# Kernel optimization log

Measured on AMD Instinct MI355X. Metric: run time of the kernel, lower is better.

The kernel has to match this reference:

```python
import jax, jax.numpy as jnp
import numpy as np

B, S, D, H = 2, 2048, 1024, 16
HEAD_DIM = D // H
WINDOW = 256
DILATION = 1
NEG = jnp.float32(-1e9)


def _build_attn_mask(seq_len):
    # Faithful port of torch _build_attn_mask for causal=True, stencil kind='local'.
    idx = jnp.arange(seq_len)
    diff = idx[None, :] - idx[:, None]  # diff[i, j] = j - i (torch diff is idx.unsqueeze(0)-idx.unsqueeze(1))
    # causal: -inf strictly above diagonal (j > i)
    mask = jnp.where(diff > 0, -jnp.inf, 0.0).astype(jnp.float32)
    # stencil allow: |diff| <= window and |diff| % dilation == 0
    cond = (jnp.abs(diff) <= WINDOW) & (jnp.abs(diff) % DILATION == 0)
    allowed = jnp.where(cond, 0.0, -jnp.inf).astype(jnp.float32)
    # torch.maximum: allow() can UNMASK causally-masked positions inside the window
    mask = jnp.maximum(mask, allowed)
    # clamp(min=-1e9)
    return jnp.maximum(mask, NEG)


def setup_inputs() -> dict:
    key = jax.random.key(0)
    k = jax.random.split(key, 5)
    return {
        "x": jax.random.normal(k[0], (B, S, D), dtype=jnp.float32),
        "in_proj_w": jax.random.normal(k[1], (3 * D, D), dtype=jnp.float32) * (D ** -0.5),
        "in_proj_b": jax.random.normal(k[2], (3 * D,), dtype=jnp.float32) * 0.02,
        "out_proj_w": jax.random.normal(k[3], (D, D), dtype=jnp.float32) * (D ** -0.5),
        "out_proj_b": jax.random.normal(k[4], (D,), dtype=jnp.float32) * 0.02,
    }


def reference(x, in_proj_w, in_proj_b, out_proj_w, out_proj_b):
    b, s, d = x.shape
    # fused qkv projection (torch nn.MultiheadAttention in_proj)
    qkv = x @ in_proj_w.T + in_proj_b  # [b, s, 3d]
    q, k, v = jnp.split(qkv, 3, axis=-1)

    def to_heads(t):
        return t.reshape(b, s, H, HEAD_DIM).transpose(0, 2, 1, 3)  # [b, h, s, hd]

    q, k, v = to_heads(q), to_heads(k), to_heads(v)
    scale = jnp.float32(HEAD_DIM) ** -0.5
    scores = jnp.einsum("bhqd,bhkd->bhqk", q * scale, k)  # [b, h, s, s]
    mask = _build_attn_mask(s)  # [s, s]
    scores = scores + mask[None, None, :, :]
    attn = jax.nn.softmax(scores, axis=-1)
    out = jnp.einsum("bhqk,bhkd->bhqd", attn, v)  # [b, h, s, hd]
    out = out.transpose(0, 2, 1, 3).reshape(b, s, d)
    return out @ out_proj_w.T + out_proj_b
```

## Files before the change

### kernel.cpp

```cpp
#include <hip/hip_runtime.h>
#include <cstddef>

#define BATCH   2
#define SEQ     2048
#define DMODEL  1024
#define NH      16
#define HDIM    64
#define WIN     256
#define MTOT    4096

typedef __bf16 bf16;
typedef __attribute__((ext_vector_type(8)))  __bf16 bf16x8;
typedef __attribute__((ext_vector_type(4)))  float  f32x4;
typedef __attribute__((ext_vector_type(16))) float  f32x16;

#define GLOAD_LDS(gp, lp) __builtin_amdgcn_global_load_lds( \
    (const __attribute__((address_space(1))) void*)(gp),    \
    (__attribute__((address_space(3))) void*)(lp), 16, 0, 0)

__device__ __forceinline__ float fast_exp2(float x) {
#if __has_builtin(__builtin_amdgcn_exp2f)
  return __builtin_amdgcn_exp2f(x);
#else
  float r; asm("v_exp_f32 %0, %1" : "=v"(r) : "v"(x)); return r;
#endif
}

__global__ __launch_bounds__(256)
void cvt_all(const float* __restrict__ x, const float* __restrict__ w1,
             const float* __restrict__ w2, bf16* __restrict__ xh,
             bf16* __restrict__ xl, bf16* __restrict__ w1h,
             bf16* __restrict__ w1l, bf16* __restrict__ w2h,
             bf16* __restrict__ w2l) {
  const int bid = blockIdx.x;
  const float* s; bf16 *hp, *lp; int base;
  if (bid < 2048)      { s = x;  hp = xh;  lp = xl;  base = bid * 2048; }
  else if (bid < 3584) { s = w1; hp = w1h; lp = w1l; base = (bid - 2048) * 2048; }
  else                 { s = w2; hp = w2h; lp = w2l; base = (bid - 3584) * 2048; }
  const int i = base + threadIdx.x * 8;
  float4 a = *(const float4*)(s + i);
  float4 c = *(const float4*)(s + i + 4);
  const float f[8] = {a.x, a.y, a.z, a.w, c.x, c.y, c.z, c.w};
  bf16x8 vh, vl;
#pragma unroll
  for (int j = 0; j < 8; ++j) {
    bf16 hh = (bf16)f[j];
    vh[j] = hh;
    vl[j] = (bf16)(f[j] - (float)hh);
  }
  *(bf16x8*)(hp + i) = vh;
  *(bf16x8*)(lp + i) = vl;
}

__global__ __launch_bounds__(256)
void gemm_qkv_fused(const bf16* __restrict__ xh, const bf16* __restrict__ xl,
                    const bf16* __restrict__ w1h, const bf16* __restrict__ w1l,
                    const float* __restrict__ b1,
                    bf16* __restrict__ Qh, bf16* __restrict__ Ql,
                    bf16* __restrict__ Kt, bf16* __restrict__ Vt) {
  __shared__ bf16 sAh[128 * 32];
  __shared__ bf16 sAl[128 * 32];
  __shared__ bf16 sBh[128 * 32];
  __shared__ bf16 sBl[128 * 32];

  const int t = threadIdx.x, w = t >> 6, lane = t & 63;
  const int ln15 = lane & 15, quad = lane >> 4;
  const int wrow = (w & 1) * 64, wcol = (w >> 1) * 64;
  const int drow = lane >> 2;
  const int dkcol = (lane & 3) * 8;
  const int bid = blockIdx.x;

  f32x4 acc[4][4];
#pragma unroll
  for (int i = 0; i < 4; ++i)
#pragma unroll
    for (int j = 0; j < 4; ++j)
#pragma unroll
      for (int r = 0; r < 4; ++r) acc[i][j][r] = 0.f;

  if (bid < 512) {
    const int bm = (bid >> 4) * 128;
    const int bnx = (bid & 15) ^ (((bid >> 8) & 1) << 3);
    const int bn = bnx * 128;
    const bool cross = (bn < 1024);

    for (int k0 = 0; k0 < DMODEL; k0 += 32) {
      __syncthreads();
#pragma unroll
      for (int half = 0; half < 2; ++half) {
        const int r = w * 32 + half * 16 + drow;
        const size_t goffA = (size_t)(bm + r) * DMODEL + k0 + dkcol;
        const size_t goffB = (size_t)(bn + r) * DMODEL + k0 + dkcol;
        const int loff = (w * 32 + half * 16) * 32;
        GLOAD_LDS(xh + goffA, sAh + loff);
        GLOAD_LDS(w1h + goffB, sBh + loff);
        if (cross) {
          GLOAD_LDS(xl + goffA, sAl + loff);
          GLOAD_LDS(w1l + goffB, sBl + loff);
        }
      }
      __syncthreads();

      bf16x8 afh[4], afl[4], bfh[4], bfl[4];
#pragma unroll
      for (int mt = 0; mt < 4; ++mt) {
        const int off = (wrow + mt * 16 + ln15) * 32 + quad * 8;
        afh[mt] = *(const bf16x8*)&sAh[off];
        if (cross) afl[mt] = *(const bf16x8*)&sAl[off];
      }
#pragma unroll
      for (int nt = 0; nt < 4; ++nt) {
        const int off = (wcol + nt * 16 + ln15) * 32 + quad * 8;
        bfh[nt] = *(const bf16x8*)&sBh[off];
        if (cross) bfl[nt] = *(const bf16x8*)&sBl[off];
      }
#pragma unroll
      for (int mt = 0; mt < 4; ++mt)
#pragma unroll
        for (int nt = 0; nt < 4; ++nt) {
          acc[mt][nt] = __builtin_amdgcn_mfma_f32_16x16x32_bf16(afh[mt], bfh[nt], acc[mt][nt], 0, 0, 0);
          if (cross) {
            acc[mt][nt] = __builtin_amdgcn_mfma_f32_16x16x32_bf16(afh[mt], bfl[nt], acc[mt][nt], 0, 0, 0);
            acc[mt][nt] = __builtin_amdgcn_mfma_f32_16x16x32_bf16(afl[mt], bfh[nt], acc[mt][nt], 0, 0, 0);
          }
        }
    }

    float bbcol[4];
#pragma unroll
    for (int nt = 0; nt < 4; ++nt) bbcol[nt] = b1[bn + wcol + nt * 16 + ln15];

#pragma unroll
    for (int mt = 0; mt < 4; ++mt)
#pragma unroll
      for (int r = 0; r < 4; ++r) {
        const size_t grow = (size_t)(bm + wrow + mt * 16 + quad * 4 + r);
#pragma unroll
        for (int nt = 0; nt < 4; ++nt) {
          const int col = bn + wcol + nt * 16 + ln15;
          const float v = acc[mt][nt][r] + bbcol[nt];
          if (col < 1024) {
            const bf16 hh = (bf16)v;
            Qh[grow * 1024 + col] = hh;
            Ql[grow * 1024 + col] = (bf16)(v - (float)hh);
          } else {
            const int btok = (int)(grow >> 11), key = (int)(grow & 2047);
            const int kt = key >> 6, kw = key & 63;
            const int hh2 = (col - 1024) >> 6, d = col & 63;
            const size_t addr = ((size_t)((btok * 16 + hh2) * 32 + kt) << 12)
                              + (((kw >> 5) * 4 + (d >> 4)) << 9)
                              + ((((d >> 3) & 1) << 5) + (kw & 31)) * 8 + (d & 7);
            Kt[addr] = (bf16)v;
          }
        }
      }
  } else {
    const int id = bid - 512;
    const int bm = (id >> 5) * 128, bn = (id & 31) * 128;
    const bf16* Ah = w1h + 2048 * 1024;
    const float* bias = b1 + 2048;

    for (int k0 = 0; k0 < DMODEL; k0 += 32) {
      __syncthreads();
#pragma unroll
      for (int half = 0; half < 2; ++half) {
        const int r = w * 32 + half * 16 + drow;
        const int loff = (w * 32 + half * 16) * 32;
        GLOAD_LDS(Ah + (size_t)(bm + r) * DMODEL + k0 + dkcol, sAh + loff);
        GLOAD_LDS(xh + (size_t)(bn + r) * DMODEL + k0 + dkcol, sBh + loff);
      }
      __syncthreads();

      bf16x8 af[4], bf[4];
#pragma unroll
      for (int mt = 0; mt < 4; ++mt)
        af[mt] = *(const bf16x8*)&sAh[(wrow + mt * 16 + ln15) * 32 + quad * 8];
#pragma unroll
      for (int nt = 0; nt < 4; ++nt)
        bf[nt] = *(const bf16x8*)&sBh[(wcol + nt * 16 + ln15) * 32 + quad * 8];
#pragma unroll
      for (int mt = 0; mt < 4; ++mt)
#pragma unroll
        for (int nt = 0; nt < 4; ++nt)
          acc[mt][nt] = __builtin_amdgcn_mfma_f32_16x16x32_bf16(af[mt], bf[nt], acc[mt][nt], 0, 0, 0);
    }

#pragma unroll
    for (int mt = 0; mt < 4; ++mt)
#pragma unroll
      for (int r = 0; r < 4; ++r) {
        const size_t grow = (size_t)(bm + wrow + mt * 16 + quad * 4 + r);
        const float brow = bias[grow];
        const int hh2 = (int)(grow >> 6), d = (int)(grow & 63);
#pragma unroll
        for (int nt = 0; nt < 4; ++nt) {
          const int col = bn + wcol + nt * 16 + ln15;
          const float v = acc[mt][nt][r] + brow;
          const int btok = col >> 11, key = col & 2047;
          const int kt = key >> 6, kw = key & 63;
          const size_t addr = ((size_t)((btok * 16 + hh2) * 32 + kt) << 12)
                            + (((d >> 5) * 4 + (kw >> 4)) << 9)
                            + ((((kw >> 3) & 1) << 5) + (d & 31)) * 8 + (kw & 7);
          Vt[addr] = (bf16)v;
        }
      }
  }
}

__global__ __launch_bounds__(256)
void gemm_out64(const bf16* __restrict__ Ah, const bf16* __restrict__ Al,
                const bf16* __restrict__ Bh, const bf16* __restrict__ Bl,
                const float* __restrict__ bias, float* __restrict__ Cf) {
  __shared__ bf16 sAh[64 * 32];
  __shared__ bf16 sAl[64 * 32];
  __shared__ bf16 sBh[64 * 32];
  __shared__ bf16 sBl[64 * 32];

  const int t = threadIdx.x, w = t >> 6, lane = t & 63;
  const int ln15 = lane & 15, quad = lane >> 4;
  const int bm = blockIdx.y * 64, bn = blockIdx.x * 64;
  const int wrow = (w & 1) * 32, wcol = (w >> 1) * 32;
  const int drow = lane >> 2;
  const int dkcol = (lane & 3) * 8;

  f32x4 acc[2][2];
#pragma unroll
  for (int i = 0; i < 2; ++i)
#pragma unroll
    for (int j = 0; j < 2; ++j)
#pragma unroll
      for (int r = 0; r < 4; ++r) acc[i][j][r] = 0.f;

  for (int k0 = 0; k0 < DMODEL; k0 += 32) {
    __syncthreads();
    {
      const int r = w * 16 + drow;
      const size_t goffA = (size_t)(bm + r) * DMODEL + k0 + dkcol;
      const size_t goffB = (size_t)(bn + r) * DMODEL + k0 + dkcol;
      const int loff = (w * 16) * 32;
      GLOAD_LDS(Ah + goffA, sAh + loff);
      GLOAD_LDS(Al + goffA, sAl + loff);
      GLOAD_LDS(Bh + goffB, sBh + loff);
      GLOAD_LDS(Bl + goffB, sBl + loff);
    }
    __syncthreads();

    bf16x8 afh[2], afl[2], bfh[2], bfl[2];
#pragma unroll
    for (int mt = 0; mt < 2; ++mt) {
      const int off = (wrow + mt * 16 + ln15) * 32 + quad * 8;
      afh[mt] = *(const bf16x8*)&sAh[off];
      afl[mt] = *(const bf16x8*)&sAl[off];
    }
#pragma unroll
    for (int nt = 0; nt < 2; ++nt) {
      const int off = (wcol + nt * 16 + ln15) * 32 + quad * 8;
      bfh[nt] = *(const bf16x8*)&sBh[off];
      bfl[nt] = *(const bf16x8*)&sBl[off];
    }
#pragma unroll
    for (int mt = 0; mt < 2; ++mt)
#pragma unroll
      for (int nt = 0; nt < 2; ++nt) {
        acc[mt][nt] = __builtin_amdgcn_mfma_f32_16x16x32_bf16(afh[mt], bfh[nt], acc[mt][nt], 0, 0, 0);
        acc[mt][nt] = __builtin_amdgcn_mfma_f32_16x16x32_bf16(afh[mt], bfl[nt], acc[mt][nt], 0, 0, 0);
        acc[mt][nt] = __builtin_amdgcn_mfma_f32_16x16x32_bf16(afl[mt], bfh[nt], acc[mt][nt], 0, 0, 0);
      }
  }

  float bbcol[2];
#pragma unroll
  for (int nt = 0; nt < 2; ++nt) bbcol[nt] = bias[bn + wcol + nt * 16 + ln15];

#pragma unroll
  for (int mt = 0; mt < 2; ++mt)
#pragma unroll
    for (int r = 0; r < 4; ++r) {
      const size_t grow = (size_t)(bm + wrow + mt * 16 + quad * 4 + r);
#pragma unroll
      for (int nt = 0; nt < 2; ++nt) {
        const int col = bn + wcol + nt * 16 + ln15;
        Cf[grow * 1024 + col] = acc[mt][nt][r] + bbcol[nt];
      }
    }
}

__global__ __launch_bounds__(64, 2)
void attn_mfma(const bf16* __restrict__ Qh, const bf16* __restrict__ Ql,
               const bf16* __restrict__ Kt, const bf16* __restrict__ Vt,
               bf16* __restrict__ Omh, bf16* __restrict__ Oml) {
  const int lane = threadIdx.x & 63;
  const int ln31 = lane & 31, half = lane >> 5;
  const int bid = blockIdx.x;
  const int j = bid & 31;
  const int bh = ((j & 7) << 2) | (j >> 3);
  const int c  = 63 - (bid >> 5);
  const int b = bh >> 4, h = bh & 15;
  const int i0w = c * 32;
  const int lim = i0w + WIN;

  __shared__ bf16 sP[32 * 72];

  bf16x8 qh[4], ql[4];
  {
    const size_t rowQ = (size_t)(b * SEQ + i0w + ln31);
#pragma unroll
    for (int ks = 0; ks < 4; ++ks) {
      bf16x8 vh = *(const bf16x8*)(Qh + rowQ * 1024 + h * 64 + ks * 16 + half * 8);
      bf16x8 vl = *(const bf16x8*)(Ql + rowQ * 1024 + h * 64 + ks * 16 + half * 8);
#pragma unroll
      for (int jj = 0; jj < 8; ++jj) {
        float f = ((float)vh[jj] + (float)vl[jj]) * 0.1803368801111204f;
        bf16 hh = (bf16)f;
        qh[ks][jj] = hh;
        ql[ks][jj] = (bf16)(f - (float)hh);
      }
    }
  }
  bf16x8 onesf;
#pragma unroll
  for (int jj = 0; jj < 8; ++jj) onesf[jj] = (ln31 == 0) ? (bf16)1.0f : (bf16)0.0f;

  f32x16 accO0, accO1, accL;
#pragma unroll
  for (int r = 0; r < 16; ++r) { accO0[r] = 0.f; accO1[r] = 0.f; accL[r] = 0.f; }

  const bf16* KtBH = Kt + ((size_t)(b * 16 + h) << 17);
  const bf16* VtBH = Vt + ((size_t)(b * 16 + h) << 17);
  const int lane8 = lane * 8;

  const int nkt = min((i0w + 31 + WIN) / 64 + 1, SEQ / 64);

  for (int kt = 0; kt < nkt; ++kt) {
    const bf16* Kb = KtBH + ((size_t)kt << 12);
    const bf16* Vb = VtBH + ((size_t)kt << 12);

    bf16x8 kf[8], vf[8];
#pragma unroll
    for (int s = 0; s < 8; ++s) {
      kf[s] = *(const bf16x8*)&Kb[(s << 9) + lane8];
      vf[s] = *(const bf16x8*)&Vb[(s << 9) + lane8];
    }

    f32x16 S0, S1;
#pragma unroll
    for (int r = 0; r < 16; ++r) { S0[r] = 0.f; S1[r] = 0.f; }
#pragma unroll
    for (int ks = 0; ks < 4; ++ks) {
      S0 = __builtin_amdgcn_mfma_f32_32x32x16_bf16(qh[ks], kf[ks], S0, 0, 0, 0);
      S0 = __builtin_amdgcn_mfma_f32_32x32x16_bf16(ql[ks], kf[ks], S0, 0, 0, 0);
      S1 = __builtin_amdgcn_mfma_f32_32x32x16_bf16(qh[ks], kf[4 + ks], S1, 0, 0, 0);
      S1 = __builtin_amdgcn_mfma_f32_32x32x16_bf16(ql[ks], kf[4 + ks], S1, 0, 0, 0);
    }

    const int j0 = kt * 64;
#pragma unroll
    for (int cc = 0; cc < 2; ++cc) {
      f32x16& S = cc ? S1 : S0;
      const int vj = j0 + cc * 32 + ln31 - lim;
      const bool may = (j0 + cc * 32 + 31) > lim;
#pragma unroll
      for (int r = 0; r < 16; ++r) {
        const int rl = (r & 3) + 8 * (r >> 2) + 4 * half;
        float pv = fast_exp2(S[r]);
        if (may && (vj > rl)) pv = 0.f;
        sP[rl * 72 + cc * 32 + ln31] = (bf16)pv;
      }
    }

#pragma unroll
    for (int ks = 0; ks < 4; ++ks) {
      bf16x8 pA = *(const bf16x8*)&sP[ln31 * 72 + ks * 16 + half * 8];
      accO0 = __builtin_amdgcn_mfma_f32_32x32x16_bf16(pA, vf[ks], accO0, 0, 0, 0);
      accO1 = __builtin_amdgcn_mfma_f32_32x32x16_bf16(pA, vf[4 + ks], accO1, 0, 0, 0);
      accL  = __builtin_amdgcn_mfma_f32_32x32x16_bf16(pA, onesf, accL, 0, 0, 0);
    }
  }

#pragma unroll
  for (int r = 0; r < 16; ++r) {
    const int rl = (r & 3) + 8 * (r >> 2) + 4 * half;
    const float lv = __shfl(accL[r], lane & 32, 64);
    const float inv = 1.0f / lv;
    const size_t grow = (size_t)(b * SEQ + i0w + rl);
    const int col0 = h * 64 + ln31;
    const float v0 = accO0[r] * inv;
    const float v1 = accO1[r] * inv;
    const bf16 h0 = (bf16)v0, h1 = (bf16)v1;
    Omh[grow * DMODEL + col0]      = h0;
    Oml[grow * DMODEL + col0]      = (bf16)(v0 - (float)h0);
    Omh[grow * DMODEL + col0 + 32] = h1;
    Oml[grow * DMODEL + col0 + 32] = (bf16)(v1 - (float)h1);
  }
}

extern "C" void kernel_launch(void* const* d_in, const int* in_sizes, int n_in,
                              void* d_out, int out_size, void* d_ws, size_t ws_size,
                              hipStream_t stream) {
  const float* x  = (const float*)d_in[0];
  const float* w1 = (const float*)d_in[1];
  const float* b1 = (const float*)d_in[2];
  const float* w2 = (const float*)d_in[3];
  const float* b2 = (const float*)d_in[4];
  float* out = (float*)d_out;

  char* ws = (char*)d_ws;
  bf16* Qh   = (bf16*)(ws + 0);
  bf16* Ql   = (bf16*)(ws + 8388608);
  bf16* Kt   = (bf16*)(ws + 16777216);
  bf16* Vt   = (bf16*)(ws + 25165824);
  bf16* xh   = (bf16*)(ws + 33554432);
  bf16* xl   = (bf16*)(ws + 41943040);
  bf16* w1h  = (bf16*)(ws + 50331648);
  bf16* w1l  = (bf16*)(ws + 56623104);
  bf16* w2h  = (bf16*)(ws + 62914560);
  bf16* w2l  = (bf16*)(ws + 65011712);
  bf16* Omh  = xh;
  bf16* Oml  = xl;

  cvt_all<<<dim3(4096), 256, 0, stream>>>(x, w1, w2, xh, xl, w1h, w1l, w2h, w2l);

  gemm_qkv_fused<<<dim3(768), 256, 0, stream>>>(
      xh, xl, w1h, w1l, b1, Qh, Ql, Kt, Vt);

  attn_mfma<<<dim3(2048), 64, 0, stream>>>(Qh, Ql, Kt, Vt, Omh, Oml);

  gemm_out64<<<dim3(16, 64), 256, 0, stream>>>(
      Omh, Oml, w2h, w2l, b2, out);
}
```

Baseline: 251.3 us.

## Split Q projection into smaller 128x64 tiles and separate K/V GEMM branches

Before, the Q and K blocks of the fused QKV GEMM shared one 128x128 tile loop, and a runtime 'cross' flag chose between three-MFMA split-bf16 work for Q and single-MFMA work for K. Now Q gets its own 128x64 tiles (512 blocks, each wave owning 32 rows) that always do the three-MFMA split, and K gets a dedicated 128x128 branch with no cross logic. The grid grows from 768 to 1024 blocks. This removes the per-block imbalance where Q blocks did three times the MFMA work of K blocks, and drops the runtime branching. The launch bound now asks for 4 blocks per CU, which limits registers, and the smaller Q tiles give less operand reuse per load.

```diff
diff --git a/kernel.cpp b/kernel.cpp
--- a/kernel.cpp
+++ b/kernel.cpp
@@ -52,7 +52,7 @@
   *(bf16x8*)(lp + i) = vl;
 }
 
-__global__ __launch_bounds__(256)
+__global__ __launch_bounds__(256, 4)
 void gemm_qkv_fused(const bf16* __restrict__ xh, const bf16* __restrict__ xl,
                     const bf16* __restrict__ w1h, const bf16* __restrict__ w1l,
                     const float* __restrict__ b1,
@@ -61,28 +61,25 @@
   __shared__ bf16 sAh[128 * 32];
   __shared__ bf16 sAl[128 * 32];
   __shared__ bf16 sBh[128 * 32];
-  __shared__ bf16 sBl[128 * 32];
+  __shared__ bf16 sBl[64 * 32];
 
   const int t = threadIdx.x, w = t >> 6, lane = t & 63;
   const int ln15 = lane & 15, quad = lane >> 4;
-  const int wrow = (w & 1) * 64, wcol = (w >> 1) * 64;
   const int drow = lane >> 2;
   const int dkcol = (lane & 3) * 8;
   const int bid = blockIdx.x;
 
-  f32x4 acc[4][4];
-#pragma unroll
-  for (int i = 0; i < 4; ++i)
-#pragma unroll
-    for (int j = 0; j < 4; ++j)
-#pragma unroll
-      for (int r = 0; r < 4; ++r) acc[i][j][r] = 0.f;
-
   if (bid < 512) {
     const int bm = (bid >> 4) * 128;
-    const int bnx = (bid & 15) ^ (((bid >> 8) & 1) << 3);
-    const int bn = bnx * 128;
-    const bool cross = (bn < 1024);
+    const int bn = (bid & 15) * 64;
+
+    f32x4 acc[2][4];
+#pragma unroll
+    for (int i = 0; i < 2; ++i)
+#pragma unroll
+      for (int j = 0; j < 4; ++j)
+#pragma unroll
+        for (int r = 0; r < 4; ++r) acc[i][j][r] = 0.f;
 
     for (int k0 = 0; k0 < DMODEL; k0 += 32) {
       __syncthreads();
@@ -90,40 +87,96 @@
       for (int half = 0; half < 2; ++half) {
         const int r = w * 32 + half * 16 + drow;
         const size_t goffA = (size_t)(bm + r) * DMODEL + k0 + dkcol;
-        const size_t goffB = (size_t)(bn + r) * DMODEL + k0 + dkcol;
         const int loff = (w * 32 + half * 16) * 32;
         GLOAD_LDS(xh + goffA, sAh + loff);
+        GLOAD_LDS(xl + goffA, sAl + loff);
+      }
+      {
+        const int r = w * 16 + drow;
+        const size_t goffB = (size_t)(bn + r) * DMODEL + k0 + dkcol;
+        const int loff = (w * 16) * 32;
         GLOAD_LDS(w1h + goffB, sBh + loff);
-        if (cross) {
-          GLOAD_LDS(xl + goffA, sAl + loff);
-          GLOAD_LDS(w1l + goffB, sBl + loff);
-        }
-      }
-      __syncthreads();
-
-      bf16x8 afh[4], afl[4], bfh[4], bfl[4];
-#pragma unroll
-      for (int mt = 0; mt < 4; ++mt) {
-        const int off = (wrow + mt * 16 + ln15) * 32 + quad * 8;
+        GLOAD_LDS(w1l + goffB, sBl + loff);
+      }
+      __syncthreads();
+
+      bf16x8 afh[2], afl[2], bfh[4], bfl[4];
+#pragma unroll
+      for (int mt = 0; mt < 2; ++mt) {
+        const int off = (w * 32 + mt * 16 + ln15) * 32 + quad * 8;
         afh[mt] = *(const bf16x8*)&sAh[off];
-        if (cross) afl[mt] = *(const bf16x8*)&sAl[off];
+        afl[mt] = *(const bf16x8*)&sAl[off];
       }
 #pragma unroll
       for (int nt = 0; nt < 4; ++nt) {
-        const int off = (wcol + nt * 16 + ln15) * 32 + quad * 8;
+        const int off = (nt * 16 + ln15) * 32 + quad * 8;
         bfh[nt] = *(const bf16x8*)&sBh[off];
-        if (cross) bfl[nt] = *(const bf16x8*)&sBl[off];
-      }
-#pragma unroll
-      for (int mt = 0; mt < 4; ++mt)
+        bfl[nt] = *(const bf16x8*)&sBl[off];
+      }
+#pragma unroll
+      for (int mt = 0; mt < 2; ++mt)
 #pragma unroll
         for (int nt = 0; nt < 4; ++nt) {
           acc[mt][nt] = __builtin_amdgcn_mfma_f32_16x16x32_bf16(afh[mt], bfh[nt], acc[mt][nt], 0, 0, 0);
-          if (cross) {
-            acc[mt][nt] = __builtin_amdgcn_mfma_f32_16x16x32_bf16(afh[mt], bfl[nt], acc[mt][nt], 0, 0, 0);
-            acc[mt][nt] = __builtin_amdgcn_mfma_f32_16x16x32_bf16(afl[mt], bfh[nt], acc[mt][nt], 0, 0, 0);
-          }
+          acc[mt][nt] = __builtin_amdgcn_mfma_f32_16x16x32_bf16(afh[mt], bfl[nt], acc[mt][nt], 0, 0, 0);
+          acc[mt][nt] = __builtin_amdgcn_mfma_f32_16x16x32_bf16(afl[mt], bfh[nt], acc[mt][nt], 0, 0, 0);
         }
+    }
+
+    float bbcol[4];
+#pragma unroll
+    for (int nt = 0; nt < 4; ++nt) bbcol[nt] = b1[bn + nt * 16 + ln15];
+
+#pragma unroll
+    for (int mt = 0; mt < 2; ++mt)
+#pragma unroll
+      for (int r = 0; r < 4; ++r) {
+        const size_t grow = (size_t)(bm + w * 32 + mt * 16 + quad * 4 + r);
+#pragma unroll
+        for (int nt = 0; nt < 4; ++nt) {
+          const int col = bn + nt * 16 + ln15;
+          const float v = acc[mt][nt][r] + bbcol[nt];
+          const bf16 hh = (bf16)v;
+          Qh[grow * 1024 + col] = hh;
+          Ql[grow * 1024 + col] = (bf16)(v - (float)hh);
+        }
+      }
+  } else if (bid < 768) {
+    const int kid = bid - 512;
+    const int bm = (kid >> 3) * 128, bn = 1024 + (kid & 7) * 128;
+    const int wrow = (w & 1) * 64, wcol = (w >> 1) * 64;
+
+    f32x4 acc[4][4];
+#pragma unroll
+    for (int i = 0; i < 4; ++i)
+#pragma unroll
+      for (int j = 0; j < 4; ++j)
+#pragma unroll
+        for (int r = 0; r < 4; ++r) acc[i][j][r] = 0.f;
+
+    for (int k0 = 0; k0 < DMODEL; k0 += 32) {
+      __syncthreads();
+#pragma unroll
+      for (int half = 0; half < 2; ++half) {
+        const int r = w * 32 + half * 16 + drow;
+        const int loff = (w * 32 + half * 16) * 32;
+        GLOAD_LDS(xh + (size_t)(bm + r) * DMODEL + k0 + dkcol, sAh + loff);
+        GLOAD_LDS(w1h + (size_t)(bn + r) * DMODEL + k0 + dkcol, sBh + loff);
+      }
+      __syncthreads();
+
+      bf16x8 af[4], bf[4];
+#pragma unroll
+      for (int mt = 0; mt < 4; ++mt)
+        af[mt] = *(const bf16x8*)&sAh[(wrow + mt * 16 + ln15) * 32 + quad * 8];
+#pragma unroll
+      for (int nt = 0; nt < 4; ++nt)
+        bf[nt] = *(const bf16x8*)&sBh[(wcol + nt * 16 + ln15) * 32 + quad * 8];
+#pragma unroll
+      for (int mt = 0; mt < 4; ++mt)
+#pragma unroll
+        for (int nt = 0; nt < 4; ++nt)
+          acc[mt][nt] = __builtin_amdgcn_mfma_f32_16x16x32_bf16(af[mt], bf[nt], acc[mt][nt], 0, 0, 0);
     }
 
     float bbcol[4];
@@ -135,30 +188,33 @@
 #pragma unroll
       for (int r = 0; r < 4; ++r) {
         const size_t grow = (size_t)(bm + wrow + mt * 16 + quad * 4 + r);
+        const int btok = (int)(grow >> 11), key = (int)(grow & 2047);
+        const int kt = key >> 6, kw = key & 63;
 #pragma unroll
         for (int nt = 0; nt < 4; ++nt) {
           const int col = bn + wcol + nt * 16 + ln15;
           const float v = acc[mt][nt][r] + bbcol[nt];
-          if (col < 1024) {
-            const bf16 hh = (bf16)v;
-            Qh[grow * 1024 + col] = hh;
-            Ql[grow * 1024 + col] = (bf16)(v - (float)hh);
-          } else {
-            const int btok = (int)(grow >> 11), key = (int)(grow & 2047);
-            const int kt = key >> 6, kw = key & 63;
-            const int hh2 = (col - 1024) >> 6, d = col & 63;
-            const size_t addr = ((size_t)((btok * 16 + hh2) * 32 + kt) << 12)
-                              + (((kw >> 5) * 4 + (d >> 4)) << 9)
-                              + ((((d >> 3) & 1) << 5) + (kw & 31)) * 8 + (d & 7);
-            Kt[addr] = (bf16)v;
-          }
+          const int hh2 = (col - 1024) >> 6, d = col & 63;
+          const size_t addr = ((size_t)((btok * 16 + hh2) * 32 + kt) << 12)
+                            + (((kw >> 5) * 4 + (d >> 4)) << 9)
+                            + ((((d >> 3) & 1) << 5) + (kw & 31)) * 8 + (d & 7);
+          Kt[addr] = (bf16)v;
         }
       }
   } else {
-    const int id = bid - 512;
-    const int bm = (id >> 5) * 128, bn = (id & 31) * 128;
+    const int vid = bid - 768;
+    const int bm = (vid >> 5) * 128, bn = (vid & 31) * 128;
+    const int wrow = (w & 1) * 64, wcol = (w >> 1) * 64;
     const bf16* Ah = w1h + 2048 * 1024;
     const float* bias = b1 + 2048;
+
+    f32x4 acc[4][4];
+#pragma unroll
+    for (int i = 0; i < 4; ++i)
+#pragma unroll
+      for (int j = 0; j < 4; ++j)
+#pragma unroll
+        for (int r = 0; r < 4; ++r) acc[i][j][r] = 0.f;
 
     for (int k0 = 0; k0 < DMODEL; k0 += 32) {
       __syncthreads();
@@ -420,7 +476,7 @@
 
   cvt_all<<<dim3(4096), 256, 0, stream>>>(x, w1, w2, xh, xl, w1h, w1l, w2h, w2l);
 
-  gemm_qkv_fused<<<dim3(768), 256, 0, stream>>>(
+  gemm_qkv_fused<<<dim3(1024), 256, 0, stream>>>(
       xh, xl, w1h, w1l, b1, Qh, Ql, Kt, Vt);
 
   attn_mfma<<<dim3(2048), 64, 0, stream>>>(Qh, Ql, Kt, Vt, Omh, Oml);
```

New measurement: 239.5 us. 4.7% less time.
